# Performance work log

Measured on AMD Instinct MI355X. Metric: run time of the kernel, lower is better.

Reference implementation:

```python
import jax, jax.numpy as jnp
import numpy as np

D_MODEL = 1024
D_STATE = 16
D_CONV = 4
EXPAND = 2
D_INNER = EXPAND * D_MODEL
DT_RANK = D_MODEL // 16  # ceil(1024/16) = 64
BSZ = 2
SEQ = 1024


def _silu(x):
    return x * jax.nn.sigmoid(x)


def _mamba(x, in_proj, conv_w, conv_b, x_proj, dt_w, dt_b, A_log, Dp, out_proj):
    """Single-direction Mamba block. x: (B, L, d_model)."""
    Bb, Ll, _ = x.shape
    xz = jnp.einsum('bld,ed->ble', x, in_proj)          # (B,L,2*d_inner)
    xi, z = jnp.split(xz, 2, axis=-1)                   # (B,L,d_inner)
    # depthwise causal conv1d over L (kernel d_conv)
    xp = jnp.pad(xi, ((0, 0), (D_CONV - 1, 0), (0, 0)))
    xc = conv_b + sum(conv_w[:, k] * xp[:, k:k + Ll, :] for k in range(D_CONV))
    xc = _silu(xc)                                      # (B,L,d_inner)
    dbl = jnp.einsum('ble,fe->blf', xc, x_proj)         # (B,L,dt_rank+2*d_state)
    dt, Bm, Cm = jnp.split(dbl, [DT_RANK, DT_RANK + D_STATE], axis=-1)
    delta = jax.nn.softplus(jnp.einsum('blr,er->ble', dt, dt_w) + dt_b)  # (B,L,d_inner)
    A = -jnp.exp(A_log)                                 # (d_inner,d_state)
    dA = jnp.exp(delta[..., None] * A)                  # (B,L,E,N)
    dBu = (delta * xc)[..., None] * Bm[:, :, None, :]   # (B,L,E,N)
    def step(h, t):
        dA_t, dBu_t, C_t = t
        h = dA_t * h + dBu_t                            # (B,E,N)
        return h, jnp.einsum('ben,bn->be', h, C_t)
    h0 = jnp.zeros((Bb, D_INNER, D_STATE), x.dtype)
    _, ys = jax.lax.scan(step, h0, (dA.transpose(1, 0, 2, 3),
                                    dBu.transpose(1, 0, 2, 3),
                                    Cm.transpose(1, 0, 2)))
    y = ys.transpose(1, 0, 2) + xc * Dp                 # skip connection
    y = y * _silu(z)                                    # gate
    return jnp.einsum('ble,de->bld', y, out_proj)


def setup_inputs() -> dict:
    key = jax.random.key(0)
    ks = jax.random.split(key, 4)
    def nrm(k, shape, s=0.02):
        return s * jax.random.normal(k, shape, dtype=jnp.float32)
    def mamba_params(kb):
        k = jax.random.split(kb, 6)
        return dict(
            in_proj=nrm(k[0], (2 * D_INNER, D_MODEL)),
            conv_w=nrm(k[1], (D_INNER, D_CONV), 0.2),
            conv_b=jnp.zeros((D_INNER,), jnp.float32),
            x_proj=nrm(k[2], (DT_RANK + 2 * D_STATE, D_INNER)),
            dt_w=nrm(k[3], (D_INNER, DT_RANK), 0.1),
            dt_b=nrm(k[4], (D_INNER,), 0.5) - 4.0,  # softplus -> dt ~ 0.018
            A_log=jnp.log(jnp.broadcast_to(jnp.arange(1, D_STATE + 1, dtype=jnp.float32), (D_INNER, D_STATE))),
            D=jnp.ones((D_INNER,), jnp.float32),
            out_proj=nrm(k[5], (D_MODEL, D_INNER)),
        )
    inp = {'x': jax.random.normal(ks[2], (BSZ, SEQ, D_MODEL), dtype=jnp.float32)}
    for name, p in (('fwd', mamba_params(ks[0])), ('bwd', mamba_params(ks[1]))):
        for kk, v in p.items():
            inp[f'{name}_{kk}'] = v
    inp['merge_w'] = nrm(ks[3], (D_MODEL, 2 * D_MODEL))
    return inp


def reference(x,
              fwd_in_proj, fwd_conv_w, fwd_conv_b, fwd_x_proj, fwd_dt_w, fwd_dt_b,
              fwd_A_log, fwd_D, fwd_out_proj,
              bwd_in_proj, bwd_conv_w, bwd_conv_b, bwd_x_proj, bwd_dt_w, bwd_dt_b,
              bwd_A_log, bwd_D, bwd_out_proj,
              merge_w):
    f = _mamba(x, fwd_in_proj, fwd_conv_w, fwd_conv_b, fwd_x_proj, fwd_dt_w,
               fwd_dt_b, fwd_A_log, fwd_D, fwd_out_proj)
    b = _mamba(jnp.flip(x, 1), bwd_in_proj, bwd_conv_w, bwd_conv_b, bwd_x_proj,
               bwd_dt_w, bwd_dt_b, bwd_A_log, bwd_D, bwd_out_proj)
    b = jnp.flip(b, 1)
    return jnp.einsum('blf,df->bld', jnp.concatenate([f, b], axis=-1), merge_w)
```

## Files before the change

kernel.cpp:

```cpp
#include <hip/hip_runtime.h>
#include <math.h>

#define BSZ 2
#define SEQ 1024
#define DM  1024
#define DI  2048
#define DS  16
#define DC  4
#define DR  64
#define NDBL 96
#define NC  32
#define LC  32
#define MM  (BSZ * SEQ)

typedef unsigned short u16;
typedef __bf16 bf16x8 __attribute__((ext_vector_type(8)));
typedef float  f32x4  __attribute__((ext_vector_type(4)));

constexpr int N4_X   = MM * DM / 4;
constexpr int N4_MW  = DM * 2 * DM / 4;
constexpr int N4_IN  = 2 * DI * DM / 4;
constexpr int N4_XP  = NDBL * DI / 4;
constexpr int N4_DT  = DI * DR / 4;
constexpr int N4_OUT = DM * DI / 4;
constexpr int N4_TOTAL = N4_X + N4_MW + 2 * (N4_IN + N4_XP + N4_DT + N4_OUT);
constexpr size_t O_XP  = (size_t)2 * DI * DM;
constexpr size_t O_DT  = O_XP + (size_t)NDBL * DI;
constexpr size_t O_OUT = O_DT + (size_t)DI * DR;
constexpr size_t WBF_SZ = O_OUT + (size_t)DM * DI;

__device__ __forceinline__ u16 f2b(float f) {
    unsigned int u = __float_as_uint(f);
    unsigned int r = (u + 0x7fffu + ((u >> 16) & 1u)) >> 16;
    return (u16)r;
}
__device__ __forceinline__ float b2f(u16 h) {
    return __uint_as_float(((unsigned int)h) << 16);
}

__device__ __forceinline__ void stf(float* p, size_t i, float v) { p[i] = v; }
__device__ __forceinline__ void stf(u16* p, size_t i, float v)   { p[i] = f2b(v); }

__device__ __forceinline__ float fexp(float x)  { return __expf(x); }
__device__ __forceinline__ float frcp(float x)  { return __builtin_amdgcn_rcpf(x); }
__device__ __forceinline__ float silu_fast(float x) {
    return x * frcp(1.f + fexp(-x));
}
__device__ __forceinline__ float softplus_fast(float x) {
    return (x > 15.f) ? x : __logf(1.f + fexp(x));
}

__device__ __forceinline__ void async16(const u16* g, u16* l) {
    __builtin_amdgcn_global_load_lds(
        (const __attribute__((address_space(1))) void*)g,
        (__attribute__((address_space(3))) void*)l, 16, 0, 0);
}

__device__ __forceinline__ int lds_slot(int row, int j) {
    return row * 4 + ((j + (row >> 1)) & 3);
}

__device__ __forceinline__ int xcd_swz(int flat, int nwg) {
    int q = nwg >> 3, r = nwg & 7;
    int x = flat & 7, i = flat >> 3;
    return (x < r ? x * (q + 1) : r * (q + 1) + (x - r) * q) + i;
}

__device__ __forceinline__ void stage8f(const float* p, u16* d) {
    float4 v0 = *(const float4*)p;
    float4 v1 = *(const float4*)(p + 4);
    ushort4 a; a.x = f2b(v0.x); a.y = f2b(v0.y); a.z = f2b(v0.z); a.w = f2b(v0.w);
    ushort4 b; b.x = f2b(v1.x); b.y = f2b(v1.y); b.z = f2b(v1.z); b.w = f2b(v1.w);
    *(ushort4*)d = a;
    *(ushort4*)(d + 4) = b;
}

__device__ __forceinline__ void stage_tile256(
    const u16* __restrict__ g, int row0, int ld, int e0, u16* lds, int t)
{
    const int wv = t >> 6, ln = t & 63;
    #pragma unroll
    for (int iss = 0; iss < 4; iss++) {
        int row = wv * 8 + iss * 2;
        const u16* src = g + (size_t)(row0 + row + (ln >> 5)) * ld
                       + e0 + (ln & 31) * 8;
        async16(src, &lds[row * 256]);
    }
}

__global__ __launch_bounds__(256) void cvt_all_kernel(
    const float* __restrict__ s0, const float* __restrict__ s1,
    const float* __restrict__ s2, const float* __restrict__ s3,
    const float* __restrict__ s4, const float* __restrict__ s5,
    const float* __restrict__ s6, const float* __restrict__ s7,
    const float* __restrict__ s8, const float* __restrict__ s9,
    u16* __restrict__ d0, u16* __restrict__ d1, u16* __restrict__ d2,
    u16* __restrict__ d3, u16* __restrict__ d4, u16* __restrict__ d5,
    u16* __restrict__ d6, u16* __restrict__ d7, u16* __restrict__ d8,
    u16* __restrict__ d9)
{
    int i = blockIdx.x * 256 + threadIdx.x;
    const float* s; u16* d;
    if (i < N4_X) { s = s0; d = d0; }
    else if ((i -= N4_X) < N4_MW) { s = s1; d = d1; }
    else if ((i -= N4_MW) < N4_IN) { s = s2; d = d2; }
    else if ((i -= N4_IN) < N4_XP) { s = s3; d = d3; }
    else if ((i -= N4_XP) < N4_DT) { s = s4; d = d4; }
    else if ((i -= N4_DT) < N4_OUT) { s = s5; d = d5; }
    else if ((i -= N4_OUT) < N4_IN) { s = s6; d = d6; }
    else if ((i -= N4_IN) < N4_XP) { s = s7; d = d7; }
    else if ((i -= N4_XP) < N4_DT) { s = s8; d = d8; }
    else if ((i -= N4_DT) < N4_OUT) { s = s9; d = d9; }
    else return;
    float4 v = ((const float4*)s)[i];
    ushort4 o; o.x = f2b(v.x); o.y = f2b(v.y); o.z = f2b(v.z); o.w = f2b(v.w);
    ((ushort4*)d)[i] = o;
}

__global__ __launch_bounds__(512) void gemm256_dual(
    const u16* __restrict__ A,
    const u16* __restrict__ Wd0, const u16* __restrict__ Wd1,
    u16* __restrict__ Cd0, u16* __restrict__ Cd1,
    int lda, int ldw, int ldc, int K)
{
    __shared__ u16 lds[65536];
    const int t    = threadIdx.x;
    const int lane = t & 63;
    const int w    = t >> 6;
    const int wr   = w >> 2;
    const int wc   = w & 3;
    const int fm   = lane & 15;
    const int q    = lane >> 4;
    const int dir  = blockIdx.z;
    const u16* W   = dir ? Wd1 : Wd0;
    u16* C         = dir ? Cd1 : Cd0;
    const int m0   = blockIdx.y * 256;
    const int n0   = blockIdx.x * 256;
    const int T    = K >> 6;

    int offA[4][2], offW[2][2];
    #pragma unroll
    for (int mi = 0; mi < 4; mi++)
        #pragma unroll
        for (int kk = 0; kk < 2; kk++) {
            int r = wr * 64 + mi * 16 + fm;
            int j = kk * 4 + q;
            offA[mi][kk] = (r * 8 + ((j + r) & 7)) * 8;
        }
    #pragma unroll
    for (int ni = 0; ni < 2; ni++)
        #pragma unroll
        for (int kk = 0; kk < 2; kk++) {
            int r = wc * 32 + ni * 16 + fm;
            int j = kk * 4 + q;
            offW[ni][kk] = (r * 8 + ((j + r) & 7)) * 8;
        }

    int sr[2], sj[2];
    #pragma unroll
    for (int p = 0; p < 2; p++) {
        int slot = p * 512 + t;
        sr[p] = slot >> 3;
        sj[p] = ((slot & 7) - sr[p]) & 7;
    }
    const int ldsWaveBase = (t & ~63) * 8;

#define STAGE(G, ld, row0, kcol, dstBase)                                    \
    { _Pragma("unroll")                                                      \
      for (int p = 0; p < 2; p++) {                                          \
          const u16* src_ = (G) + (size_t)((row0) + sr[p]) * (ld)            \
                          + (kcol) + sj[p] * 8;                              \
          async16(src_, &lds[(dstBase) + p * 4096 + ldsWaveBase]);           \
      } }

    f32x4 acc[2][2][4][2] = {};
    bf16x8 af[4][2], wf[2][2];

#define DSREAD_A(mh, cur)                                                    \
    { _Pragma("unroll")                                                      \
      for (int mi = 0; mi < 4; mi++)                                         \
          _Pragma("unroll")                                                  \
          for (int kk = 0; kk < 2; kk++)                                     \
              af[mi][kk] = *(const bf16x8*)&lds[(cur) + (mh) * 8192          \
                                                + offA[mi][kk]]; }
#define DSREAD_W(nh, cur)                                                    \
    { _Pragma("unroll")                                                      \
      for (int ni = 0; ni < 2; ni++)                                         \
          _Pragma("unroll")                                                  \
          for (int kk = 0; kk < 2; kk++)                                     \
              wf[ni][kk] = *(const bf16x8*)&lds[(cur) + 16384 + (nh) * 8192  \
                                                + offW[ni][kk]]; }
#define MFMA16(mh, nh)                                                       \
    { __builtin_amdgcn_s_setprio(1);                                         \
      _Pragma("unroll")                                                      \
      for (int mi = 0; mi < 4; mi++)                                         \
          _Pragma("unroll")                                                  \
          for (int ni = 0; ni < 2; ni++)                                     \
              _Pragma("unroll")                                              \
              for (int kk = 0; kk < 2; kk++)                                 \
                  acc[mh][nh][mi][ni] =                                      \
                      __builtin_amdgcn_mfma_f32_16x16x32_bf16(               \
                          af[mi][kk], wf[ni][kk], acc[mh][nh][mi][ni],       \
                          0, 0, 0);                                          \
      __builtin_amdgcn_s_setprio(0); }

#define WAITVM(n) asm volatile("s_waitcnt vmcnt(" #n ")" ::: "memory")
#define BAR() __builtin_amdgcn_s_barrier()

    STAGE(A, lda, m0,       0, 0);
    STAGE(W, ldw, n0,       0, 16384);
    STAGE(W, ldw, n0 + 128, 0, 16384 + 8192);
    STAGE(A, lda, m0 + 128, 0, 8192);
    WAITVM(4);
    BAR();

    for (int tt = 0; tt < T - 1; ++tt) {
        const int cur = (tt & 1) * 32768;
        const int nxt = 32768 - cur;
        const int kn  = (tt + 1) << 6;
        DSREAD_A(0, cur); DSREAD_W(0, cur);
        STAGE(A, lda, m0, kn, nxt);
        WAITVM(4);
        BAR();
        MFMA16(0, 0);
        BAR();
        DSREAD_W(1, cur);
        STAGE(W, ldw, n0, kn, nxt + 16384);
        WAITVM(4);
        BAR();
        MFMA16(0, 1);
        BAR();
        DSREAD_A(1, cur);
        STAGE(W, ldw, n0 + 128, kn, nxt + 16384 + 8192);
        BAR();
        MFMA16(1, 1);
        BAR();
        DSREAD_W(0, cur);
        STAGE(A, lda, m0 + 128, kn, nxt + 8192);
        WAITVM(4);
        BAR();
        MFMA16(1, 0);
        BAR();
    }
    {
        const int cur = ((T - 1) & 1) * 32768;
        DSREAD_A(0, cur); DSREAD_W(0, cur);
        WAITVM(2);
        BAR();
        MFMA16(0, 0);
        BAR();
        DSREAD_W(1, cur);
        WAITVM(0);
        BAR();
        MFMA16(0, 1);
        BAR();
        DSREAD_A(1, cur);
        BAR();
        MFMA16(1, 1);
        BAR();
        DSREAD_W(0, cur);
        MFMA16(1, 0);
    }
#undef STAGE
#undef DSREAD_A
#undef DSREAD_W
#undef MFMA16
#undef WAITVM
#undef BAR

    #pragma unroll
    for (int mh = 0; mh < 2; mh++)
        #pragma unroll
        for (int mi = 0; mi < 4; mi++)
            #pragma unroll
            for (int rr = 0; rr < 4; rr++) {
                int gm = m0 + mh * 128 + wr * 64 + mi * 16 + q * 4 + rr;
                int om = gm;
                if (dir == 1) {
                    om = (gm & ~(SEQ - 1)) | ((SEQ - 1) - (gm & (SEQ - 1)));
                }
                u16* crow = C + (size_t)om * ldc;
                #pragma unroll
                for (int nh = 0; nh < 2; nh++)
                    #pragma unroll
                    for (int ni = 0; ni < 2; ni++) {
                        int gn = n0 + nh * 128 + wc * 32 + ni * 16 + fm;
                        crow[gn] = f2b(acc[mh][nh][mi][ni][rr]);
                    }
            }
}

template <typename TA, typename TC, int ACT, bool DUAL, bool FLIP1, int NSPLIT,
          int BN, bool SWZ>
__global__ __launch_bounds__(256) void mfma_gemm(
    const TA* __restrict__ A0, const TA* __restrict__ A1, int lda,
    const u16* __restrict__ W0, const u16* __restrict__ W1, int ldw,
    const float* __restrict__ bias0, const float* __restrict__ bias1,
    TC* __restrict__ C0, TC* __restrict__ C1, int ldc,
    int M, int N, int K)
{
    constexpr int NF = BN / 32;
    __shared__ u16 As[2][128 * 32];
    __shared__ u16 Ws[2][BN * 32];

    int bx = blockIdx.x, by = blockIdx.y, bz = blockIdx.z;
    if (SWZ) {
        const int gx = gridDim.x, gy = gridDim.y;
        const int nwg = gx * gy * gridDim.z;
        int flat = (blockIdx.z * gy + blockIdx.y) * gx + blockIdx.x;
        flat = xcd_swz(flat, nwg);
        bx = flat % gx;
        int rest = flat / gx;
        by = rest % gy;
        bz = rest / gy;
    }

    const int z = bz;
    const int dir = DUAL ? (z / NSPLIT) : 0;
    const int split = z % NSPLIT;
    const TA* A = dir ? A1 : A0;
    const u16* W = dir ? W1 : W0;
    const float* bias = dir ? bias1 : bias0;
    TC* C = dir ? C1 : C0;
    if (NSPLIT > 1) C += (size_t)split * M * ldc;
    const int kseg = K / NSPLIT;
    const int kbeg = split * kseg;
    const int kiters = kseg / 32;

    const int t = threadIdx.x;
    const int wave = t >> 6;
    const int lane = t & 63;
    const int wm = (wave & 1) * 64;
    const int wn = (wave >> 1) * (BN / 2);
    const int fm = lane & 15;
    const int q  = lane >> 4;
    const int m0 = by * 128;
    const int n0 = bx * BN;

    auto stage_tile = [&](int k0, int b) {
        if constexpr (__is_same(TA, u16)) {
            #pragma unroll
            for (int p = 0; p < 2; p++) {
                int i = p * 256 + wave * 64 + lane;
                int r = i >> 2;
                int j = ((i & 3) - (r >> 1)) & 3;
                async16(A + (size_t)(m0 + r) * lda + k0 + j * 8,
                        &As[b][(size_t)(p * 256 + wave * 64) * 8]);
            }
        } else {
            #pragma unroll
            for (int p = 0; p < 2; p++) {
                int i = p * 256 + t;
                int r = i >> 2;
                int j = ((i & 3) - (r >> 1)) & 3;
                stage8f(A + (size_t)(m0 + r) * lda + k0 + j * 8,
                        &As[b][(size_t)i * 8]);
            }
        }
        #pragma unroll
        for (int p = 0; p < BN / 64; p++) {
            int i = p * 256 + wave * 64 + lane;
            int r = i >> 2;
            int j = ((i & 3) - (r >> 1)) & 3;
            int gr = n0 + r;
            if (gr >= N) gr = N - 1;
            async16(W + (size_t)gr * ldw + k0 + j * 8,
                    &Ws[b][(size_t)(p * 256 + wave * 64) * 8]);
        }
    };

    f32x4 acc[4][NF] = {};

    stage_tile(kbeg, 0);
    __syncthreads();

    for (int ii = 0; ii < kiters; ii++) {
        const int cur = ii & 1;
        if (ii + 1 < kiters)
            stage_tile(kbeg + (ii + 1) * 32, cur ^ 1);

        bf16x8 af[4], wf[NF];
        #pragma unroll
        for (int mi = 0; mi < 4; mi++)
            af[mi] = *(const bf16x8*)
                &As[cur][(size_t)lds_slot(wm + mi * 16 + fm, q) * 8];
        #pragma unroll
        for (int ni = 0; ni < NF; ni++)
            wf[ni] = *(const bf16x8*)
                &Ws[cur][(size_t)lds_slot(wn + ni * 16 + fm, q) * 8];
        #pragma unroll
        for (int mi = 0; mi < 4; mi++)
            #pragma unroll
            for (int ni = 0; ni < NF; ni++)
                acc[mi][ni] = __builtin_amdgcn_mfma_f32_16x16x32_bf16(
                    af[mi], wf[ni], acc[mi][ni], 0, 0, 0);

        __syncthreads();
    }

    const int rb = q * 4;
    const int cc = fm;
    #pragma unroll
    for (int mi = 0; mi < 4; mi++) {
        #pragma unroll
        for (int r = 0; r < 4; r++) {
            int gm = m0 + wm + mi * 16 + rb + r;
            int om = gm;
            if (FLIP1 && dir == 1) {
                int bb = gm / SEQ, l = gm % SEQ;
                om = bb * SEQ + (SEQ - 1 - l);
            }
            #pragma unroll
            for (int ni = 0; ni < NF; ni++) {
                int gn = n0 + wn + ni * 16 + cc;
                if (gn < N) {
                    float v = acc[mi][ni][r];
                    if (ACT == 1) v = softplus_fast(v + bias[gn]);
                    stf(C, (size_t)om * ldc + gn, v);
                }
            }
        }
    }
}

__global__ __launch_bounds__(256) void combine_dbl_kernel(
    const float* __restrict__ par, float* __restrict__ dbl)
{
    int i4 = blockIdx.x * 256 + threadIdx.x;
    const int per = (MM * NDBL) / 4;
    int dir = (i4 >= per) ? 1 : 0;
    int j4 = i4 - dir * per;
    const float* p = par + (size_t)dir * 4 * MM * NDBL;
    f32x4 s = {0.f, 0.f, 0.f, 0.f};
    #pragma unroll
    for (int k = 0; k < 4; k++)
        s += *(const f32x4*)&p[(size_t)k * MM * NDBL + (size_t)j4 * 4];
    *(f32x4*)&dbl[(size_t)dir * MM * NDBL + (size_t)j4 * 4] = s;
}

__global__ __launch_bounds__(256) void combine_out_kernel(
    const float* __restrict__ p0, float* __restrict__ out)
{
    int i4 = blockIdx.x * 256 + threadIdx.x;
    const float* p1 = p0 + (size_t)MM * DM;
    f32x4 a = *(const f32x4*)&p0[(size_t)i4 * 4];
    f32x4 b = *(const f32x4*)&p1[(size_t)i4 * 4];
    *(f32x4*)&out[(size_t)i4 * 4] = a + b;
}

__global__ __launch_bounds__(256) void conv_silu_kernel(
    const u16* __restrict__ xz,
    const float* __restrict__ cw0, const float* __restrict__ cw1,
    const float* __restrict__ cb0, const float* __restrict__ cb1,
    u16* __restrict__ xcb)
{
    int i4 = blockIdx.x * 256 + threadIdx.x;
    const int per = MM * DI / 4;
    int dir = (i4 >= per) ? 1 : 0;
    int rem = i4 - dir * per;
    int e4 = rem & (DI / 4 - 1);
    int bl = rem / (DI / 4);
    int l = bl & (SEQ - 1);
    int e = e4 * 4;
    const u16* xz_d = xz + (size_t)dir * MM * 2 * DI;
    const float* cw = dir ? cw1 : cw0;
    const float* cb = dir ? cb1 : cb0;
    f32x4 cwv[4];
    #pragma unroll
    for (int i = 0; i < 4; i++) cwv[i] = *(const f32x4*)&cw[(e + i) * DC];
    f32x4 acc = *(const f32x4*)&cb[e];
    #pragma unroll
    for (int k = 0; k < DC; k++) {
        int ll = l + k - (DC - 1);
        if (ll >= 0) {
            ushort4 xv = *(const ushort4*)&xz_d[(size_t)(bl - l + ll) * (2 * DI) + e];
            acc[0] += cwv[0][k] * b2f(xv.x);
            acc[1] += cwv[1][k] * b2f(xv.y);
            acc[2] += cwv[2][k] * b2f(xv.z);
            acc[3] += cwv[3][k] * b2f(xv.w);
        }
    }
    ushort4 o;
    #pragma unroll
    for (int i = 0; i < 4; i++) {
        float s = silu_fast(acc[i]);
        ((u16*)&o)[i] = f2b(s);
    }
    ((ushort4*)xcb)[(size_t)dir * per + rem] = o;
}

__global__ __launch_bounds__(256) void scan_pass1(
    const float* __restrict__ dbl,
    const u16*  __restrict__ xc,
    const u16*  __restrict__ delta,
    const float* __restrict__ Alog0, const float* __restrict__ Alog1,
    float* __restrict__ Qout, float* __restrict__ Dout)
{
    __shared__ float sB[LC][16];
    __shared__ u16 sD[LC * 256];
    __shared__ u16 sX[LC * 256];
    const int t = threadIdx.x;
    const int c = blockIdx.x;
    const int dir = blockIdx.z >> 1;
    const int b = blockIdx.z & 1;
    const int ey = blockIdx.y;
    const int e = ey * 256 + t;
    const int row0 = b * SEQ + c * LC;
    const float* dbl_d = dbl + (size_t)dir * MM * NDBL;
    const u16* xc_d = xc + (size_t)dir * MM * DI;
    const u16* delta_d = delta + (size_t)dir * MM * DI;
    const float* A_log = dir ? Alog1 : Alog0;
    float* Q_d = Qout + (size_t)dir * BSZ * NC * DI * DS;
    float* D_d = Dout + (size_t)dir * BSZ * NC * DI;

    stage_tile256(delta_d, row0, DI, ey * 256, sD, t);
    stage_tile256(xc_d,    row0, DI, ey * 256, sX, t);

    if (t < LC * 4) {
        int row = t >> 2, col = (t & 3) * 4;
        *(f32x4*)&sB[row][col] =
            *(const f32x4*)&dbl_d[(size_t)(row0 + row) * NDBL + DR + col];
    }

    f32x4 Aen[4], Q[4];
    #pragma unroll
    for (int g = 0; g < 4; g++) {
        f32x4 a = *(const f32x4*)&A_log[(size_t)e * DS + g * 4];
        #pragma unroll
        for (int j = 0; j < 4; j++) Aen[g][j] = -fexp(a[j]);
        Q[g] = f32x4{0.f, 0.f, 0.f, 0.f};
    }
    const float a0 = Aen[0][0];
    bool pw = true;
    #pragma unroll
    for (int g = 0; g < 4; g++)
        #pragma unroll
        for (int j = 0; j < 4; j++)
            pw = pw && (fabsf(Aen[g][j] - (float)(g * 4 + j + 1) * a0)
                        <= 1e-4f * fabsf(Aen[g][j]));
    __syncthreads();

    float dsum = 0.f;
    if (pw) {
        for (int i = 0; i < LC; i++) {
            float dv = b2f(sD[i * 256 + t]);
            float xv = b2f(sX[i * 256 + t]);
            float du = dv * xv;
            dsum += dv;
            float e1 = fexp(dv * a0);
            float e2 = e1 * e1, e3 = e2 * e1, e4 = e2 * e2;
            float e8 = e4 * e4, e12 = e8 * e4;
            float lo[4] = {e1, e2, e3, e4};
            float Eg[4] = {1.f, e4, e8, e12};
            #pragma unroll
            for (int g = 0; g < 4; g++) {
                f32x4 Bv = *(const f32x4*)&sB[i][g * 4];
                #pragma unroll
                for (int j = 0; j < 4; j++) {
                    float dA = (g == 0) ? lo[j] : Eg[g] * lo[j];
                    Q[g][j] = dA * Q[g][j] + du * Bv[j];
                }
            }
        }
    } else {
        for (int i = 0; i < LC; i++) {
            float dv = b2f(sD[i * 256 + t]);
            float xv = b2f(sX[i * 256 + t]);
            float du = dv * xv;
            dsum += dv;
            #pragma unroll
            for (int g = 0; g < 4; g++) {
                f32x4 Bv = *(const f32x4*)&sB[i][g * 4];
                #pragma unroll
                for (int j = 0; j < 4; j++) {
                    float dA = fexp(dv * Aen[g][j]);
                    Q[g][j] = dA * Q[g][j] + du * Bv[j];
                }
            }
        }
    }
    size_t base = ((size_t)(b * NC + c) * DI + e) * DS;
    #pragma unroll
    for (int g = 0; g < 4; g++)
        *(f32x4*)&Q_d[base + g * 4] = Q[g];
    D_d[(size_t)(b * NC + c) * DI + e] = dsum;
}

__global__ __launch_bounds__(256) void scan_pass2(
    const float* __restrict__ Q, const float* __restrict__ Dsum,
    const float* __restrict__ Alog0, const float* __restrict__ Alog1,
    float* __restrict__ H0)
{
    const int gid = blockIdx.x * 256 + threadIdx.x;
    const int dir = gid >> 16;
    const int loc = gid & 65535;
    const int b = loc >> 15;
    const int en = loc & (DI * DS - 1);
    const int e = en >> 4;
    const float* A_log = dir ? Alog1 : Alog0;
    const float aen = -fexp(A_log[en]);
    size_t doff = (size_t)dir * BSZ * NC * DI * DS;
    size_t doffD = (size_t)dir * BSZ * NC * DI;
    float h = 0.f;
    for (int c = 0; c < NC; c++) {
        size_t idx = doff + ((size_t)(b * NC + c) * DI * DS) + en;
        H0[idx] = h;
        float Dc = Dsum[doffD + (size_t)(b * NC + c) * DI + e];
        h = fexp(Dc * aen) * h + Q[idx];
    }
}

__global__ __launch_bounds__(256) void scan_pass3(
    const float* __restrict__ dbl,
    const u16*  __restrict__ xc,
    const u16*  __restrict__ xz,
    u16* delta_y,
    const float* __restrict__ Alog0, const float* __restrict__ Alog1,
    const float* __restrict__ Dp0, const float* __restrict__ Dp1,
    const float* __restrict__ H0)
{
    __shared__ float sBC[LC][32];
    __shared__ u16 sD[LC * 256];
    __shared__ u16 sX[LC * 256];
    __shared__ u16 sZ[LC * 256];
    const int t = threadIdx.x;
    const int c = blockIdx.x;
    const int dir = blockIdx.z >> 1;
    const int b = blockIdx.z & 1;
    const int ey = blockIdx.y;
    const int e = ey * 256 + t;
    const int row0 = b * SEQ + c * LC;
    const float* dbl_d = dbl + (size_t)dir * MM * NDBL;
    const u16* xc_d = xc + (size_t)dir * MM * DI;
    const u16* xz_d = xz + (size_t)dir * MM * 2 * DI;
    u16* dy_d = delta_y + (size_t)dir * MM * DI;
    const float* A_log = dir ? Alog1 : Alog0;
    const float* Dp = dir ? Dp1 : Dp0;
    const float* H0_d = H0 + (size_t)dir * BSZ * NC * DI * DS;

    stage_tile256(dy_d, row0, DI, ey * 256, sD, t);
    stage_tile256(xc_d, row0, DI, ey * 256, sX, t);
    stage_tile256(xz_d, row0, 2 * DI, DI + ey * 256, sZ, t);

    {
        int row = t >> 3, col = (t & 7) * 4;
        *(f32x4*)&sBC[row][col] =
            *(const f32x4*)&dbl_d[(size_t)(row0 + row) * NDBL + DR + col];
    }

    f32x4 Aen[4], h[4];
    size_t base = ((size_t)(b * NC + c) * DI + e) * DS;
    #pragma unroll
    for (int g = 0; g < 4; g++) {
        f32x4 a = *(const f32x4*)&A_log[(size_t)e * DS + g * 4];
        #pragma unroll
        for (int j = 0; j < 4; j++) Aen[g][j] = -fexp(a[j]);
        h[g] = *(const f32x4*)&H0_d[base + g * 4];
    }
    const float Dv = Dp[e];
    const float a0 = Aen[0][0];
    bool pw = true;
    #pragma unroll
    for (int g = 0; g < 4; g++)
        #pragma unroll
        for (int j = 0; j < 4; j++)
            pw = pw && (fabsf(Aen[g][j] - (float)(g * 4 + j + 1) * a0)
                        <= 1e-4f * fabsf(Aen[g][j]));
    __syncthreads();

    if (pw) {
        for (int i = 0; i < LC; i++) {
            float dv = b2f(sD[i * 256 + t]);
            float xv = b2f(sX[i * 256 + t]);
            float zv = b2f(sZ[i * 256 + t]);
            float du = dv * xv;
            float e1 = fexp(dv * a0);
            float e2 = e1 * e1, e3 = e2 * e1, e4 = e2 * e2;
            float e8 = e4 * e4, e12 = e8 * e4;
            float lo[4] = {e1, e2, e3, e4};
            float Eg[4] = {1.f, e4, e8, e12};
            f32x4 pv = {0.f, 0.f, 0.f, 0.f};
            #pragma unroll
            for (int g = 0; g < 4; g++) {
                f32x4 Bv = *(const f32x4*)&sBC[i][g * 4];
                f32x4 Cv = *(const f32x4*)&sBC[i][16 + g * 4];
                #pragma unroll
                for (int j = 0; j < 4; j++) {
                    float dA = (g == 0) ? lo[j] : Eg[g] * lo[j];
                    h[g][j] = dA * h[g][j] + du * Bv[j];
                    pv[j] += h[g][j] * Cv[j];
                }
            }
            float p = pv[0] + pv[1] + pv[2] + pv[3];
            float y = (p + xv * Dv) * silu_fast(zv);
            dy_d[(size_t)(row0 + i) * DI + e] = f2b(y);
        }
    } else {
        for (int i = 0; i < LC; i++) {
            float dv = b2f(sD[i * 256 + t]);
            float xv = b2f(sX[i * 256 + t]);
            float zv = b2f(sZ[i * 256 + t]);
            float du = dv * xv;
            f32x4 pv = {0.f, 0.f, 0.f, 0.f};
            #pragma unroll
            for (int g = 0; g < 4; g++) {
                f32x4 Bv = *(const f32x4*)&sBC[i][g * 4];
                f32x4 Cv = *(const f32x4*)&sBC[i][16 + g * 4];
                #pragma unroll
                for (int j = 0; j < 4; j++) {
                    float dA = fexp(dv * Aen[g][j]);
                    h[g][j] = dA * h[g][j] + du * Bv[j];
                    pv[j] += h[g][j] * Cv[j];
                }
            }
            float p = pv[0] + pv[1] + pv[2] + pv[3];
            float y = (p + xv * Dv) * silu_fast(zv);
            dy_d[(size_t)(row0 + i) * DI + e] = f2b(y);
        }
    }
}

extern "C" void kernel_launch(void* const* d_in, const int* in_sizes, int n_in,
                              void* d_out, int out_size, void* d_ws, size_t ws_size,
                              hipStream_t stream)
{
    const float* x = (const float*)d_in[0];
    const float* in_p[2]  = {(const float*)d_in[1],  (const float*)d_in[10]};
    const float* conv_w[2]= {(const float*)d_in[2],  (const float*)d_in[11]};
    const float* conv_b[2]= {(const float*)d_in[3],  (const float*)d_in[12]};
    const float* x_p[2]   = {(const float*)d_in[4],  (const float*)d_in[13]};
    const float* dt_w[2]  = {(const float*)d_in[5],  (const float*)d_in[14]};
    const float* dt_b[2]  = {(const float*)d_in[6],  (const float*)d_in[15]};
    const float* A_log[2] = {(const float*)d_in[7],  (const float*)d_in[16]};
    const float* Dp[2]    = {(const float*)d_in[8],  (const float*)d_in[17]};
    const float* out_p[2] = {(const float*)d_in[9],  (const float*)d_in[18]};
    const float* merge_w  = (const float*)d_in[19];
    float* out = (float*)d_out;

    float* ws = (float*)d_ws;
    float* ws_dbl = ws;
    float* ws_Q   = ws_dbl + (size_t)2 * MM * NDBL;
    float* ws_D   = ws_Q   + (size_t)2 * BSZ * NC * DI * DS;
    float* ws_H0  = ws_D   + (size_t)2 * BSZ * NC * DI;
    u16* ws_xz    = (u16*)(ws_H0 + (size_t)2 * BSZ * NC * DI * DS);
    u16* ws_delta = ws_xz    + (size_t)2 * MM * 2 * DI;
    u16* ws_xcb   = ws_delta + (size_t)2 * MM * DI;
    u16* ws_cat   = ws_xcb   + (size_t)2 * MM * DI;
    u16* ws_xbf   = ws_cat   + (size_t)MM * 2 * DM;
    u16* wbf_mw   = ws_xbf   + (size_t)MM * DM;
    u16* wbf0     = wbf_mw   + (size_t)DM * 2 * DM;
    u16* wbf1     = wbf0     + WBF_SZ;
    float* ws_par = ws_Q;

    cvt_all_kernel<<<(N4_TOTAL + 255) / 256, 256, 0, stream>>>(
        x, merge_w, in_p[0], x_p[0], dt_w[0], out_p[0],
        in_p[1], x_p[1], dt_w[1], out_p[1],
        ws_xbf, wbf_mw,
        wbf0, wbf0 + O_XP, wbf0 + O_DT, wbf0 + O_OUT,
        wbf1, wbf1 + O_XP, wbf1 + O_DT, wbf1 + O_OUT);

    gemm256_dual<<<dim3(16, 8, 2), 512, 0, stream>>>(
        ws_xbf, wbf0, wbf1,
        ws_xz, ws_xz + (size_t)MM * 2 * DI,
        DM, DM, 2 * DI, DM);

    conv_silu_kernel<<<(2 * MM * DI / 4) / 256, 256, 0, stream>>>(
        ws_xz, conv_w[0], conv_w[1], conv_b[0], conv_b[1], ws_xcb);

    mfma_gemm<u16, float, 0, true, false, 4, 64, true>
        <<<dim3(2, 16, 8), 256, 0, stream>>>(
        ws_xcb, ws_xcb + (size_t)MM * DI, DI,
        wbf0 + O_XP, wbf1 + O_XP, DI, nullptr, nullptr,
        ws_par, ws_par + (size_t)4 * MM * NDBL, NDBL, MM, NDBL, DI);
    combine_dbl_kernel<<<(2 * MM * NDBL / 4) / 256, 256, 0, stream>>>(ws_par, ws_dbl);

    mfma_gemm<float, u16, 1, true, false, 1, 64, true>
        <<<dim3(32, 16, 2), 256, 0, stream>>>(
        ws_dbl, ws_dbl + (size_t)MM * NDBL, NDBL,
        wbf0 + O_DT, wbf1 + O_DT, DR, dt_b[0], dt_b[1],
        ws_delta, ws_delta + (size_t)MM * DI, DI, MM, DI, DR);

    {
        dim3 grid(NC, DI / 256, 2 * BSZ);
        scan_pass1<<<grid, 256, 0, stream>>>(ws_dbl, ws_xcb, ws_delta,
                                             A_log[0], A_log[1], ws_Q, ws_D);
        scan_pass2<<<(2 * BSZ * DI * DS) / 256, 256, 0, stream>>>(
            ws_Q, ws_D, A_log[0], A_log[1], ws_H0);
        scan_pass3<<<grid, 256, 0, stream>>>(ws_dbl, ws_xcb, ws_xz, ws_delta,
                                             A_log[0], A_log[1], Dp[0], Dp[1], ws_H0);
    }

    mfma_gemm<u16, u16, 0, true, true, 1, 64, true>
        <<<dim3(16, 16, 2), 256, 0, stream>>>(
        ws_delta, ws_delta + (size_t)MM * DI, DI,
        wbf0 + O_OUT, wbf1 + O_OUT, DI, nullptr, nullptr,
        ws_cat, ws_cat + DM, 2 * DM, MM, DM, DI);

    mfma_gemm<u16, float, 0, false, false, 2, 64, true>
        <<<dim3(16, 16, 2), 256, 0, stream>>>(
        ws_cat, ws_cat, 2 * DM, wbf_mw, wbf_mw, 2 * DM, nullptr, nullptr,
        ws_par, ws_par, DM, MM, DM, 2 * DM);
    combine_out_kernel<<<(MM * DM / 4) / 256, 256, 0, stream>>>(ws_par, out);
}
```

Before: 328.0 us.

## Triple-buffer bf16 GEMM LDS staging with fine-grained vmcnt waits

For bf16-input GEMM instantiations, the LDS staging is switched from double to triple buffering. Two tiles are kept in flight, and the code waits only on the oldest loads with explicit s_waitcnt vmcnt counts plus raw s_barrier instead of __syncthreads. MFMA sections are also wrapped in s_setprio to favour the math waves. The aim is to hide global-to-LDS latency better, at the cost of 50% more LDS per block, which may reduce occupancy. The hand-counted vmcnt values must match the exact number of issued loads per stage, otherwise the kernel reads stale data.

```diff
diff --git a/kernel.cpp b/kernel.cpp
--- a/kernel.cpp
+++ b/kernel.cpp
@@ -64,6 +64,21 @@
     int q = nwg >> 3, r = nwg & 7;
     int x = flat & 7, i = flat >> 3;
     return (x < r ? x * (q + 1) : r * (q + 1) + (x - r) * q) + i;
+}
+
+template <int N> __device__ __forceinline__ void waitvm() {
+    static_assert(N == 0 || N == 3 || N == 4 || N == 6 || N == 8, "");
+    if constexpr (N == 0) asm volatile("s_waitcnt vmcnt(0)" ::: "memory");
+    else if constexpr (N == 3) asm volatile("s_waitcnt vmcnt(3)" ::: "memory");
+    else if constexpr (N == 4) asm volatile("s_waitcnt vmcnt(4)" ::: "memory");
+    else if constexpr (N == 6) asm volatile("s_waitcnt vmcnt(6)" ::: "memory");
+    else if constexpr (N == 8) asm volatile("s_waitcnt vmcnt(8)" ::: "memory");
+}
+
+__device__ __forceinline__ void barf() {
+    asm volatile("" ::: "memory");
+    __builtin_amdgcn_s_barrier();
+    asm volatile("" ::: "memory");
 }
 
 __device__ __forceinline__ void stage8f(const float* p, u16* d) {
@@ -300,8 +315,8 @@
     int M, int N, int K)
 {
     constexpr int NF = BN / 32;
-    __shared__ u16 As[2][128 * 32];
-    __shared__ u16 Ws[2][BN * 32];
+    __shared__ u16 As[3][128 * 32];
+    __shared__ u16 Ws[3][BN * 32];
 
     int bx = blockIdx.x, by = blockIdx.y, bz = blockIdx.z;
     if (SWZ) {
@@ -371,14 +386,7 @@
 
     f32x4 acc[4][NF] = {};
 
-    stage_tile(kbeg, 0);
-    __syncthreads();
-
-    for (int ii = 0; ii < kiters; ii++) {
-        const int cur = ii & 1;
-        if (ii + 1 < kiters)
-            stage_tile(kbeg + (ii + 1) * 32, cur ^ 1);
-
+    auto compute = [&](int cur) {
         bf16x8 af[4], wf[NF];
         #pragma unroll
         for (int mi = 0; mi < 4; mi++)
@@ -388,14 +396,48 @@
         for (int ni = 0; ni < NF; ni++)
             wf[ni] = *(const bf16x8*)
                 &Ws[cur][(size_t)lds_slot(wn + ni * 16 + fm, q) * 8];
+        __builtin_amdgcn_s_setprio(1);
         #pragma unroll
         for (int mi = 0; mi < 4; mi++)
             #pragma unroll
             for (int ni = 0; ni < NF; ni++)
                 acc[mi][ni] = __builtin_amdgcn_mfma_f32_16x16x32_bf16(
                     af[mi], wf[ni], acc[mi][ni], 0, 0, 0);
-
+        __builtin_amdgcn_s_setprio(0);
+    };
+
+    if constexpr (__is_same(TA, u16)) {
+        constexpr int L = 2 + BN / 64;
+        stage_tile(kbeg, 0);
+        stage_tile(kbeg + 32, 1);
+        int cur = 0;
+        for (int ii = 0; ii + 2 < kiters; ii++) {
+            int nb = cur + 2; if (nb >= 3) nb -= 3;
+            stage_tile(kbeg + (ii + 2) * 32, nb);
+            waitvm<2 * L>();
+            barf();
+            compute(cur);
+            barf();
+            cur = (cur == 2) ? 0 : cur + 1;
+        }
+        waitvm<L>();
+        barf();
+        compute(cur);
+        barf();
+        cur = (cur == 2) ? 0 : cur + 1;
+        waitvm<0>();
+        barf();
+        compute(cur);
+    } else {
+        stage_tile(kbeg, 0);
         __syncthreads();
+        for (int ii = 0; ii < kiters; ii++) {
+            const int cur = ii & 1;
+            if (ii + 1 < kiters)
+                stage_tile(kbeg + (ii + 1) * 32, cur ^ 1);
+            compute(cur);
+            __syncthreads();
+        }
     }
 
     const int rb = q * 4;
```

After: 335.7 us. 2.3% more time.
